# Kernel tuning notes

Hardware: AMD Instinct MI355X
Metric: run time of the kernel (lower is better)

Reference implementation:

```python
import jax, jax.numpy as jnp
import numpy as np

WIN_H = 3
WIN_W = 3
DILATION = 1
CUT = 0.0  # module hard-codes self.cut = 0
EPS = 1e-12  # torch F.normalize eps


def _l2norm(x):
    # L2-normalize over channel dim (dim=1), matching torch.nn.functional.normalize
    n = jnp.sqrt(jnp.sum(x * x, axis=1, keepdims=True))
    return x / jnp.maximum(n, EPS)


def setup_inputs() -> dict:
    key = jax.random.key(0)
    k1, k2 = jax.random.split(key)
    B, C, H, W = 4, 128, 192, 256
    image = jax.random.normal(k1, (B, C, H, W), dtype=jnp.float32)
    event = jax.random.normal(k2, (B, C, H, W), dtype=jnp.float32)
    return {"image": image, "event": event}


def reference(image, event):
    B, C, H, W = image.shape
    img = _l2norm(image)
    evt = _l2norm(event)
    p = DILATION
    imgp = jnp.pad(img, ((0, 0), (0, 0), (p, p), (p, p)))
    evtp = jnp.pad(evt, ((0, 0), (0, 0), (p, p), (p, p)))
    # Unfold ordering: reshape(B, C, K, H, W) with K positions row-major over (i, j).
    # affinity_k(p) = sum_c img_shift_k(p) * evt_shift_k(p)  -> avoid im2col blowup,
    # compute per-offset shifted dot products instead.
    affs = []
    for i in range(WIN_H):
        for j in range(WIN_W):
            oi, oj = i * DILATION, j * DILATION
            a = jnp.sum(
                imgp[:, :, oi:oi + H, oj:oj + W] * evtp[:, :, oi:oi + H, oj:oj + W],
                axis=1,
            )  # [B, H, W]
            affs.append(a)
    affinity = jnp.stack(affs, axis=1)  # [B, K=9, H, W]
    # affinity[affinity < cut] = cut  with cut == 0
    return jnp.maximum(affinity, CUT)
```

## Files before the change

kernel.cpp:

```cpp
#include <hip/hip_runtime.h>

#define BB 4
#define CC 128
#define HH 192
#define WW 256
#define HW (HH * WW)

__global__ __launch_bounds__(256) void dotnorm_kernel(
    const float* __restrict__ img, const float* __restrict__ evt,
    float* __restrict__ D)
{
    const int blk = blockIdx.x;
    const int tid = threadIdx.x;
    const int qx  = tid & 15;
    const int cz  = tid >> 4;
    const int seg = blk & 3;
    const int row = blk >> 2;
    const int b   = row / HH;
    const int h   = row - b * HH;
    const int w0  = seg * 64 + (qx << 2);
    const int base0 = b * CC * HW + h * WW + w0;
    const int cbase = cz * 8;

    float4 aii = make_float4(0.f, 0.f, 0.f, 0.f);
    float4 aee = make_float4(0.f, 0.f, 0.f, 0.f);
    float4 aie = make_float4(0.f, 0.f, 0.f, 0.f);

    #pragma unroll
    for (int c = 0; c < 8; ++c) {
        const float4 iv = *reinterpret_cast<const float4*>(img + base0 + (cbase + c) * HW);
        const float4 ev = *reinterpret_cast<const float4*>(evt + base0 + (cbase + c) * HW);
        aii.x += iv.x * iv.x; aii.y += iv.y * iv.y; aii.z += iv.z * iv.z; aii.w += iv.w * iv.w;
        aee.x += ev.x * ev.x; aee.y += ev.y * ev.y; aee.z += ev.z * ev.z; aee.w += ev.w * ev.w;
        aie.x += iv.x * ev.x; aie.y += iv.y * ev.y; aie.z += iv.z * ev.z; aie.w += iv.w * ev.w;
    }

    __shared__ float s_ii[16][64];
    __shared__ float s_ee[16][64];
    __shared__ float s_ie[16][64];
    const int p4 = qx << 2;
    s_ii[cz][p4 + 0] = aii.x; s_ii[cz][p4 + 1] = aii.y; s_ii[cz][p4 + 2] = aii.z; s_ii[cz][p4 + 3] = aii.w;
    s_ee[cz][p4 + 0] = aee.x; s_ee[cz][p4 + 1] = aee.y; s_ee[cz][p4 + 2] = aee.z; s_ee[cz][p4 + 3] = aee.w;
    s_ie[cz][p4 + 0] = aie.x; s_ie[cz][p4 + 1] = aie.y; s_ie[cz][p4 + 2] = aie.z; s_ie[cz][p4 + 3] = aie.w;
    __syncthreads();

    if (tid < 64) {
        float ii = 0.f, ee = 0.f, ie = 0.f;
        #pragma unroll
        for (int k = 0; k < 16; ++k) {
            ii += s_ii[k][tid];
            ee += s_ee[k][tid];
            ie += s_ie[k][tid];
        }
        const float ni = fmaxf(sqrtf(ii), 1e-12f);
        const float ne = fmaxf(sqrtf(ee), 1e-12f);
        D[row * WW + seg * 64 + tid] = ie / (ni * ne);
    }
}

__global__ __launch_bounds__(256) void gather_kernel(
    const float* __restrict__ D, float* __restrict__ out)
{
    const int idx = blockIdx.x * 256 + threadIdx.x;
    const int qx   = idx & 63;
    const int rest = idx >> 6;
    const int h    = rest % HH;
    const int bk   = rest / HH;
    const int k    = bk % 9;
    const int b    = bk / 9;
    const int i    = k / 3;
    const int j    = k - 3 * i;
    const int w0   = qx << 2;

    const int y  = h + i - 1;
    const bool vy = (y >= 0) && (y < HH);
    const int rowbase = (b * HH + y) * WW;

    float4 o;
    float* op = &o.x;
    #pragma unroll
    for (int e = 0; e < 4; ++e) {
        const int x = w0 + e + j - 1;
        const float v = (vy && x >= 0 && x < WW) ? D[rowbase + x] : 0.0f;
        op[e] = fmaxf(v, 0.0f);
    }
    *reinterpret_cast<float4*>(out + (size_t)idx * 4) = o;
}

extern "C" void kernel_launch(void* const* d_in, const int* in_sizes, int n_in,
                              void* d_out, int out_size, void* d_ws, size_t ws_size,
                              hipStream_t stream) {
    const float* img = (const float*)d_in[0];
    const float* evt = (const float*)d_in[1];
    float* out = (float*)d_out;
    float* D   = (float*)d_ws;

    dotnorm_kernel<<<BB * HH * 4, 256, 0, stream>>>(img, evt, D);
    gather_kernel<<<(BB * 9 * HH * WW / 4) / 256, 256, 0, stream>>>(D, out);
}
```

Before: 38.86 us.

## Fuse gather into dot kernel via scatter stores plus output memset

Removes the intermediate D buffer and the second gather kernel. Each thread that computes a pixel's normalized dot product now scatters it, clamped at zero, with nontemporal stores into up to nine output positions. A memset beforehand zeros the border entries the scatter never writes. This saves the D write/read round trip and one launch, but adds a full memset pass over the output. The scatter stores are scalar and strided across nine planes, so they are less coalesced than the gather's float4 writes.

New measurement: 41.96 us. 1.08x slower.

```diff
diff --git a/kernel.cpp b/kernel.cpp
--- a/kernel.cpp
+++ b/kernel.cpp
@@ -6,9 +6,9 @@
 #define WW 256
 #define HW (HH * WW)
 
-__global__ __launch_bounds__(256) void dotnorm_kernel(
+__global__ __launch_bounds__(256) void dotscatter_kernel(
     const float* __restrict__ img, const float* __restrict__ evt,
-    float* __restrict__ D)
+    float* __restrict__ out)
 {
     const int blk = blockIdx.x;
     const int tid = threadIdx.x;
@@ -54,37 +54,24 @@
         }
         const float ni = fmaxf(sqrtf(ii), 1e-12f);
         const float ne = fmaxf(sqrtf(ee), 1e-12f);
-        D[row * WW + seg * 64 + tid] = ie / (ni * ne);
+        const float dc = fmaxf(ie / (ni * ne), 0.0f);
+
+        const int w  = seg * 64 + tid;
+        const int ob = b * 9;
+        #pragma unroll
+        for (int i = 0; i < 3; ++i) {
+            const int th = h + 1 - i;
+            if (th < 0 || th >= HH) continue;
+            #pragma unroll
+            for (int j = 0; j < 3; ++j) {
+                const int tw = w + 1 - j;
+                if (tw >= 0 && tw < WW) {
+                    __builtin_nontemporal_store(
+                        dc, out + (((ob + i * 3 + j) * HH + th) * WW + tw));
+                }
+            }
+        }
     }
-}
-
-__global__ __launch_bounds__(256) void gather_kernel(
-    const float* __restrict__ D, float* __restrict__ out)
-{
-    const int idx = blockIdx.x * 256 + threadIdx.x;
-    const int qx   = idx & 63;
-    const int rest = idx >> 6;
-    const int h    = rest % HH;
-    const int bk   = rest / HH;
-    const int k    = bk % 9;
-    const int b    = bk / 9;
-    const int i    = k / 3;
-    const int j    = k - 3 * i;
-    const int w0   = qx << 2;
-
-    const int y  = h + i - 1;
-    const bool vy = (y >= 0) && (y < HH);
-    const int rowbase = (b * HH + y) * WW;
-
-    float4 o;
-    float* op = &o.x;
-    #pragma unroll
-    for (int e = 0; e < 4; ++e) {
-        const int x = w0 + e + j - 1;
-        const float v = (vy && x >= 0 && x < WW) ? D[rowbase + x] : 0.0f;
-        op[e] = fmaxf(v, 0.0f);
-    }
-    *reinterpret_cast<float4*>(out + (size_t)idx * 4) = o;
 }
 
 extern "C" void kernel_launch(void* const* d_in, const int* in_sizes, int n_in,
@@ -93,8 +80,8 @@
     const float* img = (const float*)d_in[0];
     const float* evt = (const float*)d_in[1];
     float* out = (float*)d_out;
-    float* D   = (float*)d_ws;
 
-    dotnorm_kernel<<<BB * HH * 4, 256, 0, stream>>>(img, evt, D);
-    gather_kernel<<<(BB * 9 * HH * WW / 4) / 256, 256, 0, stream>>>(D, out);
+    hipMemsetAsync(out, 0, (size_t)out_size * sizeof(float), stream);
+
+    dotscatter_kernel<<<BB * HH * 4, 256, 0, stream>>>(img, evt, out);
 }
```
